# Optimization experiments

Measured on AMD Instinct MI355X. Metric: run time of the kernel, lower is better.

The kernel has to match this reference:

```python
import jax, jax.numpy as jnp
import numpy as np

MASK_FILL = -99999.0  # value used by masked_fill_ in the torch source


def setup_inputs() -> dict:
    key = jax.random.key(0)
    k1, k2, k3, k4, k5, k6, k7 = jax.random.split(key, 7)
    B, S, H = 8, 2048, 1024
    query = jax.random.normal(k1, (B, S, H), dtype=jnp.float32)
    key_t = jax.random.normal(k2, (B, S, H), dtype=jnp.float32)
    value = jax.random.normal(k3, (B, S, H), dtype=jnp.float32)
    mask = jax.random.randint(k4, (B, S), 0, 2, dtype=jnp.int32)
    s = 1.0 / np.sqrt(H)
    Wq = jax.random.uniform(k5, (H, H), dtype=jnp.float32, minval=-s, maxval=s)
    Wk = jax.random.uniform(k6, (H, H), dtype=jnp.float32, minval=-s, maxval=s)
    Wv = jax.random.uniform(k7, (H, H), dtype=jnp.float32, minval=-s, maxval=s)
    return {"query": query, "key": key_t, "value": value,
            "Wq": Wq, "Wk": Wk, "Wv": Wv, "mask": mask}


def reference(query, key, value, Wq, Wk, Wv, mask):
    # Linear(h,h,bias=False): y = x @ W.T
    q = jnp.einsum('bsh,oh->bso', query, Wq)
    k = jnp.einsum('bsh,oh->bso', key, Wk)
    v = jnp.einsum('bsh,oh->bso', value, Wv)
    # score[b,i,j] = q[b,i,:] . k[b,j,:]  (NO 1/sqrt(d) scaling in source)
    score = jnp.einsum('bqh,bkh->bqk', q, k)
    # mask: [B, S_k] -> [B, 1, S_k]; positions where mask==0 get MASK_FILL
    m = mask[:, None, :]
    score = jnp.where(m == 0, jnp.float32(MASK_FILL), score)
    attn = jax.nn.softmax(score, axis=-1)
    context = jnp.einsum('bqk,bkh->bqh', attn, v)
    return context
```

## Files before the change

kernel.cpp:

```cpp
#include <hip/hip_runtime.h>
#include <hip/hip_fp16.h>
#include <math.h>

typedef _Float16 f16;
typedef _Float16 f16x4 __attribute__((ext_vector_type(4)));
typedef _Float16 f16x8 __attribute__((ext_vector_type(8)));
typedef float f32x4 __attribute__((ext_vector_type(4)));
typedef float f32x4e __attribute__((ext_vector_type(4)));

#define GLOAD_LDS16(g, l)                                                                  \
    __builtin_amdgcn_global_load_lds((const __attribute__((address_space(1))) void*)(g),   \
                                     (__attribute__((address_space(3))) void*)(l), 16, 0, 0)

__device__ __forceinline__ void cast16(const float* __restrict__ src, f16* __restrict__ dst,
                                       long long i)
{
    const f32x4e* sp = (const f32x4e*)(src + i * 16);
    f32x4e a = __builtin_nontemporal_load(sp + 0);
    f32x4e b = __builtin_nontemporal_load(sp + 1);
    f32x4e c = __builtin_nontemporal_load(sp + 2);
    f32x4e d4 = __builtin_nontemporal_load(sp + 3);
    f16x8 lo = {(f16)a[0], (f16)a[1], (f16)a[2], (f16)a[3],
                (f16)b[0], (f16)b[1], (f16)b[2], (f16)b[3]};
    f16x8 hi = {(f16)c[0], (f16)c[1], (f16)c[2], (f16)c[3],
                (f16)d4[0], (f16)d4[1], (f16)d4[2], (f16)d4[3]};
    f16x8* dp = (f16x8*)(dst + i * 16);
    dp[0] = lo;
    dp[1] = hi;
}

__global__ __launch_bounds__(256) void prep_w_kernel(const float* __restrict__ Wq,
                                                     const float* __restrict__ Wk,
                                                     const float* __restrict__ Wv,
                                                     f16* __restrict__ dA,
                                                     f16* __restrict__ dB,
                                                     f16* __restrict__ dC)
{
    __shared__ f16 tile[64][72];
    const int z = blockIdx.z;
    const int t = threadIdx.x;
    if (z == 2) {
        const long long i = (long long)(blockIdx.y * 16 + blockIdx.x) * 256 + t;
        cast16(Wv, dC, i);
        return;
    }
    const float* src = z ? Wk : Wq;
    f16* dst = z ? dB : dA;
    const int h0 = blockIdx.x * 64, o0 = blockIdx.y * 64;
    const int r = t >> 2, c = (t & 3) * 16;
    const float* sp = src + (long long)(o0 + r) * 1024 + h0 + c;
    float4 v0 = *(const float4*)(sp + 0);
    float4 v1 = *(const float4*)(sp + 4);
    float4 v2 = *(const float4*)(sp + 8);
    float4 v3 = *(const float4*)(sp + 12);
    *(f16x4*)&tile[r][c]      = (f16x4){(f16)v0.x, (f16)v0.y, (f16)v0.z, (f16)v0.w};
    *(f16x4*)&tile[r][c + 4]  = (f16x4){(f16)v1.x, (f16)v1.y, (f16)v1.z, (f16)v1.w};
    *(f16x4*)&tile[r][c + 8]  = (f16x4){(f16)v2.x, (f16)v2.y, (f16)v2.z, (f16)v2.w};
    *(f16x4*)&tile[r][c + 12] = (f16x4){(f16)v3.x, (f16)v3.y, (f16)v3.z, (f16)v3.w};
    __syncthreads();
    f16 buf[16];
#pragma unroll
    for (int j = 0; j < 16; j++) buf[j] = tile[c + j][r];
    f16* dp = dst + (long long)(h0 + r) * 1024 + o0 + c;
    *(f16x8*)(dp)     = *(f16x8*)&buf[0];
    *(f16x8*)(dp + 8) = *(f16x8*)&buf[8];
}

__global__ __launch_bounds__(256) void fused_cast_m_kernel(
    const float* __restrict__ Xk, const float* __restrict__ Xv,
    f16* __restrict__ dXk, f16* __restrict__ dXv,
    const f16* __restrict__ whA, const f16* __restrict__ whB, f16* __restrict__ whD)
{
    __shared__ __align__(16) f16 msmem[128 * 32 * 2];
    const int z = blockIdx.z;
    const int tid = threadIdx.x;
    if (z == 0) { cast16(Xk, dXk, (long long)blockIdx.x * 256 + tid); return; }
    if (z == 1) { cast16(Xv, dXv, (long long)blockIdx.x * 256 + tid); return; }
    if (blockIdx.x >= 64) return;

    const int b = blockIdx.x;
    const int by = b >> 3, bx = b & 7;
    const char* pA = (const char*)(whA + (long long)by * 128 * 1024);
    const char* pB = (const char*)(whB + (long long)bx * 128 * 1024);
    const int w = tid >> 6, l = tid & 63;
    const int wr = w >> 1, wc = w & 1;
    f32x4 acc[4][4];
#pragma unroll
    for (int i = 0; i < 4; i++)
#pragma unroll
        for (int j = 0; j < 4; j++) acc[i][j] = (f32x4){0.f, 0.f, 0.f, 0.f};
    const int lr = l & 15, lkb = (l >> 4) * 16;

    for (int t = 0; t < 32; ++t) {
        const long long kb = (long long)t * 64;
#pragma unroll
        for (int i = 0; i < 2; i++) {
            const int c = i * 256 + tid;
            const int row = c >> 2;
            const int col = ((c & 3) * 16) ^ ((row & 3) << 4);
            GLOAD_LDS16(pA + (long long)row * 2048 + kb + col, &msmem[(long long)c * 8]);
            GLOAD_LDS16(pB + (long long)row * 2048 + kb + col, &msmem[4096 + (long long)c * 8]);
        }
        __syncthreads();
        f16x8 af[4], bf[4];
#pragma unroll
        for (int f = 0; f < 4; f++) {
            const int ra = wr * 64 + f * 16 + lr;
            const int rb = wc * 64 + f * 16 + lr;
            af[f] = *(const f16x8*)((const char*)&msmem[0] + ra * 64 + (lkb ^ ((ra & 3) << 4)));
            bf[f] = *(const f16x8*)((const char*)&msmem[4096] + rb * 64 + (lkb ^ ((rb & 3) << 4)));
        }
#pragma unroll
        for (int fq = 0; fq < 4; fq++)
#pragma unroll
            for (int fc = 0; fc < 4; fc++)
                acc[fq][fc] = __builtin_amdgcn_mfma_f32_16x16x32_f16(af[fq], bf[fc], acc[fq][fc], 0, 0, 0);
        __syncthreads();
    }
    const int rowl = (l >> 4) * 4;
#pragma unroll
    for (int fq = 0; fq < 4; fq++)
#pragma unroll
        for (int fc = 0; fc < 4; fc++)
#pragma unroll
            for (int i = 0; i < 4; i++)
                whD[(long long)(by * 128 + wr * 64 + fq * 16 + rowl + i) * 1024 +
                    bx * 128 + wc * 64 + fc * 16 + lr] = (f16)acc[fq][fc][i];
}

template <int OUTF16, int TRANSC, int XQCAST>
__global__ __launch_bounds__(512, 2) void gemm_nt_k(
    const f16* __restrict__ Ab, const f16* __restrict__ Bb, void* __restrict__ Cb,
    int K, int lda, int ldb, int ldc,
    long long sA, long long sB, long long sC, int gx,
    const float* __restrict__ xq_src, f16* __restrict__ xq_dst)
{
    __shared__ __align__(16) f16 smem[256 * 64 + 128 * 64];
    constexpr int B_OFF_E = 256 * 64;
    constexpr int B_OFF_B = B_OFF_E * 2;

    const int tid = threadIdx.x;
    if (XQCAST) {
        if (blockIdx.z == 1) { cast16(xq_src, xq_dst, (long long)blockIdx.x * 512 + tid); return; }
        if (blockIdx.x >= 512) return;
    }

    const int nwg = XQCAST ? 512 : gridDim.x;
    const int swz = (blockIdx.x & 7) * (nwg >> 3) + (blockIdx.x >> 3);
    const int bx = swz % gx, by = swz / gx;

    const int z = XQCAST ? 0 : blockIdx.z;
    const char* pA = (const char*)(Ab + z * sA + (long long)by * 256 * lda);
    const char* pB = (const char*)(Bb + z * sB + (long long)bx * 128 * ldb);
    const long long lda2 = (long long)lda * 2, ldb2 = (long long)ldb * 2;

    const int w = tid >> 6, l = tid & 63;
    const int wr = w >> 1, wc = w & 1;

    f32x4 acc[4][4];
#pragma unroll
    for (int i = 0; i < 4; i++)
#pragma unroll
        for (int j = 0; j < 4; j++) acc[i][j] = (f32x4){0.f, 0.f, 0.f, 0.f};

    const int lr = l & 15;
    const int lkb = (l >> 4) * 16;

#define FRAG_A16(row, kbyte)                                                              \
    (*(const f16x8*)((const char*)&smem[0] + ((row) * 128) + ((kbyte) ^ (((row) & 7) << 4))))
#define FRAG_B(row, kbyte)                                                                \
    (*(const f16x8*)((const char*)&smem[0] + B_OFF_B + ((row) * 128) + ((kbyte) ^ (((row) & 7) << 4))))

    const int nt = K >> 6;
    for (int t = 0; t < nt; ++t) {
        const long long kb = (long long)t * 128;
#pragma unroll
        for (int i = 0; i < 4; i++) {
            const int c = i * 512 + tid;
            const int row = c >> 3;
            const int col = ((c & 7) * 16) ^ ((row & 7) << 4);
            GLOAD_LDS16(pA + (long long)row * lda2 + kb + col, &smem[(long long)c * 8]);
        }
#pragma unroll
        for (int i = 0; i < 2; i++) {
            const int c = i * 512 + tid;
            const int row = c >> 3;
            const int col = ((c & 7) * 16) ^ ((row & 7) << 4);
            GLOAD_LDS16(pB + (long long)row * ldb2 + kb + col, &smem[B_OFF_E + (long long)c * 8]);
        }
        __syncthreads();

        f16x8 bf[4][2], af[4][2];
#pragma unroll
        for (int fc = 0; fc < 4; fc++)
#pragma unroll
            for (int ks = 0; ks < 2; ks++)
                bf[fc][ks] = FRAG_B(wc * 64 + fc * 16 + lr, ks * 64 + lkb);
#pragma unroll
        for (int fq = 0; fq < 4; fq++)
#pragma unroll
            for (int ks = 0; ks < 2; ks++)
                af[fq][ks] = FRAG_A16(wr * 64 + fq * 16 + lr, ks * 64 + lkb);

#pragma unroll
        for (int fq = 0; fq < 4; fq++)
#pragma unroll
            for (int fc = 0; fc < 4; fc++)
#pragma unroll
                for (int ks = 0; ks < 2; ks++)
                    acc[fq][fc] = __builtin_amdgcn_mfma_f32_16x16x32_f16(
                        af[fq][ks], bf[fc][ks], acc[fq][fc], 0, 0, 0);

        __syncthreads();
    }
#undef FRAG_A16
#undef FRAG_B

    const int row_l = (l >> 4) * 4;
    const long long gr0 = (long long)by * 256 + wr * 64;
    const int gc0 = bx * 128 + wc * 64;

    if (TRANSC) {
        const long long blk_r0 = (long long)by * 256;
        const int b = (int)(blk_r0 >> 11);
        const int s_base = (int)(blk_r0 & 2047);
        f16* vTp = (f16*)Cb + (long long)b * 1024 * 2048;
#pragma unroll
        for (int h = 0; h < 2; h++) {
            __syncthreads();
            if ((wr >> 1) == h) {
                const int s64 = (wr & 1) * 64;
#pragma unroll
                for (int fq = 0; fq < 4; fq++)
#pragma unroll
                    for (int fc = 0; fc < 4; fc++)
#pragma unroll
                        for (int i = 0; i < 4; i++)
                            smem[(wc * 64 + fc * 16 + lr) * 136 + s64 + fq * 16 + row_l + i] =
                                (f16)acc[fq][fc][i];
            }
            __syncthreads();
#pragma unroll
            for (int j = 0; j < 4; j++) {
                const int c = j * 512 + tid;
                const int o = c >> 4, s8 = (c & 15) * 8;
                f16x8 vv = *(const f16x8*)&smem[o * 136 + s8];
                *(f16x8*)&vTp[((long long)(bx * 128 + o)) * 2048 + s_base + h * 128 + s8] = vv;
            }
        }
    } else if (OUTF16) {
        f16* C = (f16*)Cb + z * sC;
#pragma unroll
        for (int fq = 0; fq < 4; fq++)
#pragma unroll
            for (int fc = 0; fc < 4; fc++)
#pragma unroll
                for (int i = 0; i < 4; i++)
                    C[(gr0 + fq * 16 + row_l + i) * ldc + gc0 + fc * 16 + lr] = (f16)acc[fq][fc][i];
    } else {
        float* C = (float*)Cb + z * sC;
#pragma unroll
        for (int fq = 0; fq < 4; fq++)
#pragma unroll
            for (int fc = 0; fc < 4; fc++)
#pragma unroll
                for (int i = 0; i < 4; i++)
                    __builtin_nontemporal_store(
                        acc[fq][fc][i],
                        &C[(gr0 + fq * 16 + row_l + i) * ldc + gc0 + fc * 16 + lr]);
    }
}

__device__ __forceinline__ float wred_max(float v) {
#pragma unroll
    for (int o = 32; o > 0; o >>= 1) v = fmaxf(v, __shfl_xor(v, o));
    return v;
}
__device__ __forceinline__ float wred_sum(float v) {
#pragma unroll
    for (int o = 32; o > 0; o >>= 1) v += __shfl_xor(v, o);
    return v;
}

__global__ __launch_bounds__(256) void softmax_kernel(f16* __restrict__ Sm, const int* __restrict__ mask)
{
    const long long row = blockIdx.x;
    const int b = (int)(row >> 11);
    f16* Srow = Sm + row * 2048;
    const int* mrow = mask + b * 2048;
    const int t = threadIdx.x;
    const int w = t >> 6, l = t & 63;

    f16x8 sv = *(const f16x8*)(Srow + t * 8);
    int4 m0 = *(const int4*)(mrow + t * 8);
    int4 m1 = *(const int4*)(mrow + t * 8 + 4);
    int mk[8] = {m0.x, m0.y, m0.z, m0.w, m1.x, m1.y, m1.z, m1.w};
    float v[8];
#pragma unroll
    for (int j = 0; j < 8; j++) v[j] = (float)sv[j];

    float mx = -INFINITY;
#pragma unroll
    for (int j = 0; j < 8; j++) if (mk[j]) mx = fmaxf(mx, v[j]);
    mx = wred_max(mx);
    __shared__ float redm[4], reds[4];
    if (l == 0) redm[w] = mx;
    __syncthreads();
    mx = fmaxf(fmaxf(redm[0], redm[1]), fmaxf(redm[2], redm[3]));

    if (mx == -INFINITY) {
        const f16 u = (f16)(1.0f / 2048.0f);
        f16x8 pv;
#pragma unroll
        for (int j = 0; j < 8; j++) pv[j] = u;
        *(f16x8*)(Srow + t * 8) = pv;
        return;
    }

    float e[8];
    float s = 0.f;
#pragma unroll
    for (int j = 0; j < 8; j++) { e[j] = mk[j] ? expf(v[j] - mx) : 0.f; s += e[j]; }
    s = wred_sum(s);
    if (l == 0) reds[w] = s;
    __syncthreads();
    s = reds[0] + reds[1] + reds[2] + reds[3];
    const float inv = 1.0f / s;
    f16x8 pv;
#pragma unroll
    for (int j = 0; j < 8; j++) pv[j] = (f16)(e[j] * inv);
    *(f16x8*)(Srow + t * 8) = pv;
}

extern "C" void kernel_launch(void* const* d_in, const int* in_sizes, int n_in,
                              void* d_out, int out_size, void* d_ws, size_t ws_size,
                              hipStream_t stream)
{
    const float* query = (const float*)d_in[0];
    const float* keyi  = (const float*)d_in[1];
    const float* value = (const float*)d_in[2];
    const float* Wq    = (const float*)d_in[3];
    const float* Wk    = (const float*)d_in[4];
    const float* Wv    = (const float*)d_in[5];
    const int*   mask  = (const int*)d_in[6];
    float* out = (float*)d_out;

    const long long SH = (long long)8 * 2048 * 1024;
    f16* slot0 = (f16*)d_ws;
    f16* slot1 = slot0 + SH;
    f16* slot2 = slot0 + 2 * SH;
    f16* slot3 = slot0 + 3 * SH;
    f16* slot4 = slot0 + 4 * SH;
    const long long M1 = 1024 * 1024;
    f16* whA = slot1;
    f16* whB = slot1 + M1;
    f16* whC = slot1 + 2 * M1;
    f16* whD = slot1 + 3 * M1;
    f16* Pb  = slot0;

    const long long zero = 0;

    prep_w_kernel<<<dim3(16, 16, 3), 256, 0, stream>>>(Wq, Wk, Wv, whA, whB, whC);
    fused_cast_m_kernel<<<dim3(4096, 1, 3), 256, 0, stream>>>(
        keyi, value, slot0, slot3, whA, whB, whD);
    gemm_nt_k<1, 1, 0><<<dim3(512, 1, 1), 512, 0, stream>>>(
        slot3, whC, (void*)slot4, 1024, 1024, 1024, 2048, zero, zero, zero, 8,
        nullptr, nullptr);
    gemm_nt_k<1, 0, 1><<<dim3(2048, 1, 2), 512, 0, stream>>>(
        slot0, whD, (void*)slot3, 1024, 1024, 1024, 1024, zero, zero, zero, 8,
        query, slot2);
    gemm_nt_k<1, 0, 0><<<dim3(128, 1, 8), 512, 0, stream>>>(
        slot2, slot3, (void*)Pb, 1024, 1024, 1024, 2048,
        (long long)2048 * 1024, (long long)2048 * 1024, (long long)2048 * 2048, 16,
        nullptr, nullptr);
    softmax_kernel<<<dim3(16384), 256, 0, stream>>>(Pb, mask);
    gemm_nt_k<0, 0, 0><<<dim3(64, 1, 8), 512, 0, stream>>>(
        Pb, slot4, (void*)out, 2048, 2048, 2048, 1024,
        (long long)2048 * 2048, (long long)1024 * 2048, (long long)2048 * 1024, 8,
        nullptr, nullptr);
}
```

Baseline: 314.4 us.

## Add 256x256-tile pipelined GEMM kernel for score and context matmuls

Adds a new NT GEMM kernel with 256x256 output tiles per 512-thread block, using double-buffered LDS filled by direct global-to-LDS loads and an XOR swizzle. The K loop is split into phases that interleave the next tile's loads with MFMA work, using explicit barriers, vmcnt waits and setprio. The QK^T score GEMM and the attention-times-V GEMM are switched to this kernel with half the grid size. The larger tiles aim to raise arithmetic intensity and cut global traffic, at the cost of more registers and LDS (128 KB), which limits each CU to one block and reduces the block count per GEMM.

```diff
diff --git a/kernel.cpp b/kernel.cpp
--- a/kernel.cpp
+++ b/kernel.cpp
@@ -271,6 +271,149 @@
     }
 }
 
+template <int OUTF16>
+__global__ __launch_bounds__(512, 1) void gemm_nt_256(
+    const f16* __restrict__ Ab, const f16* __restrict__ Bb, void* __restrict__ Cb,
+    int K, int lda, int ldb, int ldc,
+    long long sA, long long sB, long long sC, int gx)
+{
+    __shared__ __align__(16) f16 AS[2][2][128 * 64];
+    __shared__ __align__(16) f16 BS[2][2][128 * 64];
+
+    const int nwg = gridDim.x;
+    const int swz = (blockIdx.x & 7) * (nwg >> 3) + (blockIdx.x >> 3);
+    const int bx = swz % gx, by = swz / gx;
+    const int z = blockIdx.z;
+    const char* pA = (const char*)(Ab + z * sA + (long long)by * 256 * lda);
+    const char* pB = (const char*)(Bb + z * sB + (long long)bx * 256 * ldb);
+    const long long lda2 = (long long)lda * 2, ldb2 = (long long)ldb * 2;
+
+    const int tid = threadIdx.x;
+    const int w = tid >> 6, l = tid & 63;
+    const int wr = w >> 2, wc = w & 3;
+
+    const int sr0 = tid >> 3;
+    const int sr1 = 64 + (tid >> 3);
+    const int sc0 = ((tid & 7) * 16) ^ ((sr0 & 7) << 4);
+    const int sc1 = ((tid & 7) * 16) ^ ((sr1 & 7) << 4);
+
+#define STAGE_A(buf, h, t)                                                                 \
+    do {                                                                                   \
+        GLOAD_LDS16(pA + (long long)((h) * 128 + sr0) * lda2 + (long long)(t) * 128 + sc0, \
+                    &AS[buf][h][(long long)tid * 8]);                                      \
+        GLOAD_LDS16(pA + (long long)((h) * 128 + sr1) * lda2 + (long long)(t) * 128 + sc1, \
+                    &AS[buf][h][(long long)(512 + tid) * 8]);                              \
+    } while (0)
+#define STAGE_B(buf, h, t)                                                                 \
+    do {                                                                                   \
+        GLOAD_LDS16(pB + (long long)((h) * 128 + sr0) * ldb2 + (long long)(t) * 128 + sc0, \
+                    &BS[buf][h][(long long)tid * 8]);                                      \
+        GLOAD_LDS16(pB + (long long)((h) * 128 + sr1) * ldb2 + (long long)(t) * 128 + sc1, \
+                    &BS[buf][h][(long long)(512 + tid) * 8]);                              \
+    } while (0)
+
+#define FRAG_A(buf, r, kbyte)                                                              \
+    (*(const f16x8*)((const char*)&AS[buf][(r) >> 7][0] + ((r) & 127) * 128 +              \
+                     ((kbyte) ^ (((r) & 7) << 4))))
+#define FRAG_Bf(buf, r, kbyte)                                                             \
+    (*(const f16x8*)((const char*)&BS[buf][(r) >> 7][0] + ((r) & 127) * 128 +              \
+                     ((kbyte) ^ (((r) & 7) << 4))))
+
+    f32x4 acc[8][4];
+#pragma unroll
+    for (int i = 0; i < 8; i++)
+#pragma unroll
+        for (int j = 0; j < 4; j++) acc[i][j] = (f32x4){0.f, 0.f, 0.f, 0.f};
+
+    const int lr = l & 15;
+    const int lkb = (l >> 4) * 16;
+
+#define PHASE(buf, p, STAGECODE, VMCODE)                                                   \
+    do {                                                                                   \
+        if ((p) == 0) {                                                                    \
+            _Pragma("unroll") for (int fc = 0; fc < 4; fc++)                               \
+            _Pragma("unroll") for (int ks = 0; ks < 2; ks++)                               \
+                bf[fc][ks] = FRAG_Bf(buf, wc * 64 + fc * 16 + lr, ks * 64 + lkb);          \
+        }                                                                                  \
+        f16x8 af[2][2];                                                                    \
+        _Pragma("unroll") for (int fr = 0; fr < 2; fr++)                                   \
+        _Pragma("unroll") for (int ks = 0; ks < 2; ks++)                                   \
+            af[fr][ks] = FRAG_A(buf, wr * 128 + (p) * 32 + fr * 16 + lr, ks * 64 + lkb);   \
+        STAGECODE;                                                                         \
+        __builtin_amdgcn_s_barrier();                                                      \
+        __builtin_amdgcn_sched_barrier(0);                                                 \
+        __builtin_amdgcn_s_setprio(1);                                                     \
+        _Pragma("unroll") for (int fr = 0; fr < 2; fr++)                                   \
+        _Pragma("unroll") for (int fc = 0; fc < 4; fc++)                                   \
+        _Pragma("unroll") for (int ks = 0; ks < 2; ks++)                                   \
+            acc[(p) * 2 + fr][fc] = __builtin_amdgcn_mfma_f32_16x16x32_f16(                \
+                af[fr][ks], bf[fc][ks], acc[(p) * 2 + fr][fc], 0, 0, 0);                   \
+        __builtin_amdgcn_s_setprio(0);                                                     \
+        VMCODE;                                                                            \
+        __builtin_amdgcn_s_barrier();                                                      \
+        __builtin_amdgcn_sched_barrier(0);                                                 \
+    } while (0)
+
+    const int nt = K >> 6;
+    const int niter = nt >> 1;
+
+    STAGE_A(0, 0, 0); STAGE_A(0, 1, 0);
+    STAGE_B(0, 0, 0); STAGE_B(0, 1, 0);
+    STAGE_B(1, 0, 1); STAGE_B(1, 1, 1);
+    asm volatile("s_waitcnt vmcnt(4)" ::: "memory");
+    __builtin_amdgcn_s_barrier();
+    __builtin_amdgcn_sched_barrier(0);
+
+    for (int i = 0; i < niter; ++i) {
+        const int t1 = 2 * i + 1, t2 = 2 * i + 2, t3 = 2 * i + 3;
+        const bool fs = (t2 < nt);
+        f16x8 bf[4][2];
+        PHASE(0, 0, { STAGE_A(1, 0, t1); }, {});
+        PHASE(0, 1, { STAGE_A(1, 1, t1); }, {});
+        PHASE(0, 2, { if (fs) STAGE_B(0, 0, t2); }, {});
+        PHASE(0, 3, { if (fs) STAGE_B(0, 1, t2); },
+              {
+                  if (fs) asm volatile("s_waitcnt vmcnt(4)" ::: "memory");
+                  else    asm volatile("s_waitcnt vmcnt(0)" ::: "memory");
+              });
+        PHASE(1, 0, { if (fs) STAGE_A(0, 0, t2); }, {});
+        PHASE(1, 1, { if (fs) STAGE_A(0, 1, t2); }, {});
+        PHASE(1, 2, { if (fs) STAGE_B(1, 0, t3); }, {});
+        PHASE(1, 3, { if (fs) STAGE_B(1, 1, t3); },
+              { if (fs) asm volatile("s_waitcnt vmcnt(4)" ::: "memory"); });
+    }
+#undef PHASE
+#undef STAGE_A
+#undef STAGE_B
+#undef FRAG_A
+#undef FRAG_Bf
+
+    const int row_l = (l >> 4) * 4;
+    const long long gr0 = (long long)by * 256 + wr * 128;
+    const int gc0 = bx * 256 + wc * 64;
+    if (OUTF16) {
+        f16* C = (f16*)Cb + z * sC;
+#pragma unroll
+        for (int fq = 0; fq < 8; fq++)
+#pragma unroll
+            for (int fc = 0; fc < 4; fc++)
+#pragma unroll
+                for (int i = 0; i < 4; i++)
+                    C[(gr0 + fq * 16 + row_l + i) * ldc + gc0 + fc * 16 + lr] = (f16)acc[fq][fc][i];
+    } else {
+        float* C = (float*)Cb + z * sC;
+#pragma unroll
+        for (int fq = 0; fq < 8; fq++)
+#pragma unroll
+            for (int fc = 0; fc < 4; fc++)
+#pragma unroll
+                for (int i = 0; i < 4; i++)
+                    __builtin_nontemporal_store(
+                        acc[fq][fc][i],
+                        &C[(gr0 + fq * 16 + row_l + i) * ldc + gc0 + fc * 16 + lr]);
+    }
+}
+
 __device__ __forceinline__ float wred_max(float v) {
 #pragma unroll
     for (int o = 32; o > 0; o >>= 1) v = fmaxf(v, __shfl_xor(v, o));
@@ -369,13 +512,11 @@
     gemm_nt_k<1, 0, 1><<<dim3(2048, 1, 2), 512, 0, stream>>>(
         slot0, whD, (void*)slot3, 1024, 1024, 1024, 1024, zero, zero, zero, 8,
         query, slot2);
-    gemm_nt_k<1, 0, 0><<<dim3(128, 1, 8), 512, 0, stream>>>(
+    gemm_nt_256<1><<<dim3(64, 1, 8), 512, 0, stream>>>(
         slot2, slot3, (void*)Pb, 1024, 1024, 1024, 2048,
-        (long long)2048 * 1024, (long long)2048 * 1024, (long long)2048 * 2048, 16,
-        nullptr, nullptr);
+        (long long)2048 * 1024, (long long)2048 * 1024, (long long)2048 * 2048, 8);
     softmax_kernel<<<dim3(16384), 256, 0, stream>>>(Pb, mask);
-    gemm_nt_k<0, 0, 0><<<dim3(64, 1, 8), 512, 0, stream>>>(
+    gemm_nt_256<0><<<dim3(32, 1, 8), 512, 0, stream>>>(
         Pb, slot4, (void*)out, 2048, 2048, 2048, 1024,
-        (long long)2048 * 2048, (long long)1024 * 2048, (long long)2048 * 1024, 8,
-        nullptr, nullptr);
-}
+        (long long)2048 * 2048, (long long)1024 * 2048, (long long)2048 * 1024, 4);
+}
```

New measurement: 334.4 us. 6.3% more time.
